# Performance work log

Measured on AMD Instinct MI355X. Metric: run time of the kernel, lower is better.

## Reference

```python
import jax, jax.numpy as jnp
import numpy as np

CONF_THRES = 0.25   # NMS.conf
IOU_THRES = 0.45    # NMS.iou
MAX_NMS = 1024      # fixed candidate count so greedy NMS is jit-compatible
IMG = 640.0


def setup_inputs() -> dict:
    key = jax.random.key(0)
    k0, k1, k2, k3, k4 = jax.random.split(key, 5)
    B, N = 32, 25200
    cxcy = jax.random.uniform(k0, (B, N, 2), dtype=jnp.float32) * IMG
    wh = jax.random.uniform(k1, (B, N, 2), dtype=jnp.float32) * 80.0 + 2.0
    obj = jax.random.uniform(k2, (B, N, 1), dtype=jnp.float32)
    lmk = jax.random.uniform(k3, (B, N, 10), dtype=jnp.float32) * IMG
    cls = jax.random.uniform(k4, (B, N, 1), dtype=jnp.float32)
    # layout: [cx, cy, w, h, obj, 10 landmark coords, 1 class score]
    prediction = jnp.concatenate([cxcy, wh, obj, lmk, cls], axis=2)
    return {"prediction": prediction}


def xywh2xyxy(x):
    cx, cy, w, h = x[:, 0], x[:, 1], x[:, 2], x[:, 3]
    return jnp.stack([cx - w / 2, cy - h / 2, cx + w / 2, cy + h / 2], axis=1)


def pairwise_iou(b):  # b: [K,4] xyxy -> [K,K]
    area = (b[:, 2] - b[:, 0]) * (b[:, 3] - b[:, 1])
    lt = jnp.maximum(b[:, None, :2], b[None, :, :2])
    rb = jnp.minimum(b[:, None, 2:], b[None, :, 2:])
    wh = jnp.clip(rb - lt, 0.0)
    inter = wh[..., 0] * wh[..., 1]
    return inter / (area[:, None] + area[None, :] - inter + 1e-7)


def _nms_image(pred):  # pred: [N,16]
    obj = pred[:, 4]
    score = pred[:, 15] * obj  # x[:,15:] *= x[:,4:5]; nc==1 -> single class, j==0
    valid = (obj > CONF_THRES) & (score > CONF_THRES)  # xc filter + conf filter
    s = jnp.where(valid, score, -1.0)
    top_s, idx = jax.lax.top_k(s, MAX_NMS)  # score-sorted candidates (greedy NMS order)
    x = pred[idx]  # [K,16]
    box = xywh2xyxy(x[:, :4])
    vmask = top_s > 0.0  # valid candidates (invalid slots carry score -1)
    # class offset c = j*4096 is identically 0 since nc==1 -> skip
    iou = pairwise_iou(box)  # [K,K]
    rng = jnp.arange(MAX_NMS)

    def step(keep, i):
        sup = keep[i] & (iou[i] > IOU_THRES) & (rng > i)
        return keep & ~sup, None

    keep, _ = jax.lax.scan(step, vmask, rng)
    det = jnp.concatenate(
        [box, top_s[:, None], x[:, 5:15], jnp.zeros((MAX_NMS, 1), pred.dtype)], axis=1
    )  # [K,16] = box(4) | conf(1) | landmarks(10) | class(1)=0
    return det * keep[:, None].astype(det.dtype), keep


def reference(prediction):
    # Fixed-shape analogue of the per-image ragged output: detections padded to
    # MAX_NMS rows per image (zeroed where suppressed) plus a keep mask.
    det, keep = jax.vmap(_nms_image)(prediction)
    return det, keep
```

## Files before the change

### kernel.cpp

```cpp
#include <hip/hip_runtime.h>
#include <stdint.h>

#define NB 32
#define NN 25200
#define NN4 6300
#define TOPK 1024
#define NF 16
#define CONF 0.25f
#define IOU_T 0.45f
#define NBIN 4096
#define CAP 2048
#define KEY_BASE 0xBE800001u

__device__ __forceinline__ uint32_t score_key(float obj, float cls) {
  float score = __fmul_rn(cls, obj);
  bool valid = (obj > CONF) && (score > CONF);
  float s = valid ? score : -1.0f;
  uint32_t u = __float_as_uint(s);
  return (u & 0x80000000u) ? ~u : (u | 0x80000000u);
}

__device__ __forceinline__ uint64_t shfl_xor_u64(uint64_t v, int m) {
  uint32_t lo = __shfl_xor((uint32_t)v, m, 64);
  uint32_t hi = __shfl_xor((uint32_t)(v >> 32), m, 64);
  return ((uint64_t)hi << 32) | lo;
}

__global__ void k_keys(const float* __restrict__ pred, uint32_t* __restrict__ keys,
                       uint32_t* __restrict__ cnt) {
  if (blockIdx.x == 0 && threadIdx.x < NB) cnt[threadIdx.x] = 0u;
  int g = blockIdx.x * blockDim.x + threadIdx.x;
  if (g >= NB * NN) return;
  const float* row = pred + (size_t)g * NF;
  keys[g] = score_key(row[4], row[15]);
}

__global__ __launch_bounds__(1024) void k_select(const float* __restrict__ pred,
                                                 const uint32_t* __restrict__ keys,
                                                 int* __restrict__ sel,
                                                 float4* __restrict__ boxv,
                                                 float* __restrict__ arv,
                                                 uint32_t* __restrict__ vb) {
  int b = blockIdx.x;
  int tid = threadIdx.x;
  int lane = tid & 63, wid = tid >> 6;
  const uint4* kb4 = (const uint4*)(keys + (size_t)b * NN);
  __shared__ uint32_t hist[NBIN];
  __shared__ uint64_t ent[CAP];
  __shared__ uint32_t wsum[16];
  __shared__ uint32_t sh_bin;
  __shared__ uint32_t sh_cnt;
  #pragma unroll
  for (int k = 0; k < 4; ++k) hist[tid + 1024 * k] = 0;
  ent[tid] = 0; ent[tid + 1024] = 0;
  if (tid == 0) { sh_cnt = 0; sh_bin = 0; }
  __syncthreads();

  uint4 kreg[7];
  #pragma unroll
  for (int k = 0; k < 7; ++k) {
    int i = tid + k * 1024;
    if (i < NN4) {
      kreg[k] = kb4[i];
      uint32_t kv[4] = {kreg[k].x, kreg[k].y, kreg[k].z, kreg[k].w};
      #pragma unroll
      for (int c = 0; c < 4; ++c) {
        uint32_t key = kv[c];
        if (key >= KEY_BASE) {
          uint32_t bin = (key - KEY_BASE) >> 12;
          if (bin > NBIN - 1) bin = NBIN - 1;
          atomicAdd(&hist[bin], 1u);
        }
      }
    }
  }
  __syncthreads();

  uint32_t h[4]; uint32_t s = 0;
  #pragma unroll
  for (int k = 0; k < 4; ++k) { h[k] = hist[NBIN - 1 - (4 * tid + k)]; s += h[k]; }
  uint32_t my = s;
  #pragma unroll
  for (int d = 1; d < 64; d <<= 1) {
    uint32_t v = __shfl_up(s, d, 64);
    if (lane >= d) s += v;
  }
  if (lane == 63) wsum[wid] = s;
  __syncthreads();
  uint32_t base = 0;
  for (int w = 0; w < wid; ++w) base += wsum[w];
  uint32_t cum = base + s - my;
  #pragma unroll
  for (int k = 0; k < 4; ++k) {
    if (cum < TOPK && cum + h[k] >= TOPK) sh_bin = (uint32_t)(NBIN - 1 - (4 * tid + k));
    cum += h[k];
  }
  __syncthreads();
  uint32_t thr = KEY_BASE + (sh_bin << 12);

  #pragma unroll
  for (int k = 0; k < 7; ++k) {
    int i = tid + k * 1024;
    if (i < NN4) {
      uint32_t kv[4] = {kreg[k].x, kreg[k].y, kreg[k].z, kreg[k].w};
      #pragma unroll
      for (int c = 0; c < 4; ++c) {
        uint32_t key = kv[c];
        if (key >= thr) {
          uint32_t p = atomicAdd(&sh_cnt, 1u);
          if (p < CAP) ent[p] = ((uint64_t)key << 32) | (uint32_t)(~(uint32_t)(4 * i + c));
        }
      }
    }
  }
  __syncthreads();

  uint64_t v0 = ent[tid], v1 = ent[tid + 1024];
  for (unsigned kk = 2; kk <= CAP; kk <<= 1) {
    for (unsigned j = kk >> 1; j > 0; j >>= 1) {
      if (j == 1024) {
        uint64_t mx = v0 > v1 ? v0 : v1;
        uint64_t mn = v0 > v1 ? v1 : v0;
        v0 = mx; v1 = mn;
      } else if (j >= 64) {
        __syncthreads();
        ent[tid] = v0; ent[tid + 1024] = v1;
        __syncthreads();
        uint64_t p0 = ent[tid ^ j], p1 = ent[(tid ^ j) + 1024];
        bool low = ((tid & j) == 0);
        bool d0 = ((tid & kk) == 0);
        bool d1 = (((tid + 1024) & kk) == 0);
        v0 = (low != d0) ? (v0 < p0 ? v0 : p0) : (v0 > p0 ? v0 : p0);
        v1 = (low != d1) ? (v1 < p1 ? v1 : p1) : (v1 > p1 ? v1 : p1);
      } else {
        uint64_t p0 = shfl_xor_u64(v0, (int)j);
        uint64_t p1 = shfl_xor_u64(v1, (int)j);
        bool low = ((tid & j) == 0);
        bool d0 = ((tid & kk) == 0);
        bool d1 = (((tid + 1024) & kk) == 0);
        v0 = (low != d0) ? (v0 < p0 ? v0 : p0) : (v0 > p0 ? v0 : p0);
        v1 = (low != d1) ? (v1 < p1 ? v1 : p1) : (v1 > p1 ? v1 : p1);
      }
    }
  }
  uint32_t key = (uint32_t)(v0 >> 32);
  uint32_t n = ~(uint32_t)(v0 & 0xFFFFFFFFu);
  if (n >= NN) n = 0;
  sel[(size_t)b * TOPK + tid] = (int)n;

  bool valid = key >= KEY_BASE;
  uint64_t bal = __ballot(valid);
  if (lane == 0) {
    vb[(size_t)b * 32 + 2 * wid] = (uint32_t)bal;
    vb[(size_t)b * 32 + 2 * wid + 1] = (uint32_t)(bal >> 32);
  }

  {
    const float4* row = (const float4*)(pred + ((size_t)b * NN + n) * NF);
    float4 r0 = row[0];
    float hw = __fmul_rn(r0.z, 0.5f), hh = __fmul_rn(r0.w, 0.5f);
    float x1 = __fsub_rn(r0.x, hw), y1 = __fsub_rn(r0.y, hh);
    float x2 = __fadd_rn(r0.x, hw), y2 = __fadd_rn(r0.y, hh);
    boxv[(size_t)b * TOPK + tid] = make_float4(x1, y1, x2, y2);
    arv[(size_t)b * TOPK + tid] = __fmul_rn(__fsub_rn(x2, x1), __fsub_rn(y2, y1));
  }
}

__global__ __launch_bounds__(1024, 4) void k_maskscan(const float* __restrict__ pred,
                                                      const int* __restrict__ sel,
                                                      const float4* __restrict__ boxv,
                                                      const float* __restrict__ arv,
                                                      const uint32_t* __restrict__ vb,
                                                      uint32_t* __restrict__ mask,
                                                      uint32_t* __restrict__ cnt,
                                                      float* __restrict__ det,
                                                      float* __restrict__ keep_out) {
  int b = blockIdx.x;
  int sblk = blockIdx.y;
  int tid = threadIdx.x;
  int rg = tid & 31;
  int cc = tid >> 5;
  __shared__ uint32_t smask[32 * 1024];
  float* bx1 = (float*)smask;
  float* by1 = bx1 + TOPK;
  float* bx2 = by1 + TOPK;
  float* by2 = bx2 + TOPK;
  float* bar = by2 + TOPK;

  {
    float4 bb = boxv[(size_t)b * TOPK + tid];
    bx1[tid] = bb.x; by1[tid] = bb.y; bx2[tid] = bb.z; by2[tid] = bb.w;
    bar[tid] = arv[(size_t)b * TOPK + tid];
  }
  __syncthreads();
  int i0 = sblk * 128 + rg * 4;
  int iw = i0 >> 5;
  uint32_t wreg[4] = {0u, 0u, 0u, 0u};
  if (cc >= iw) {
    float rx1[4], ry1[4], rx2[4], ry2[4], rar[4];
    #pragma unroll
    for (int k = 0; k < 4; ++k) {
      rx1[k] = bx1[i0 + k]; ry1[k] = by1[i0 + k];
      rx2[k] = bx2[i0 + k]; ry2[k] = by2[i0 + k]; rar[k] = bar[i0 + k];
    }
    for (int jj = 0; jj < 32; ++jj) {
      int j = cc * 32 + jj;
      float cx1 = bx1[j], cy1 = by1[j], cx2 = bx2[j], cy2 = by2[j], car = bar[j];
      #pragma unroll
      for (int k = 0; k < 4; ++k) {
        float lx = fmaxf(rx1[k], cx1);
        float ly = fmaxf(ry1[k], cy1);
        float rx = fminf(rx2[k], cx2);
        float ry = fminf(ry2[k], cy2);
        float wd = fmaxf(__fsub_rn(rx, lx), 0.0f);
        float ht = fmaxf(__fsub_rn(ry, ly), 0.0f);
        float inter = __fmul_rn(wd, ht);
        float den = __fadd_rn(__fsub_rn(__fadd_rn(rar[k], car), inter), 1e-7f);
        float iou = __fdiv_rn(inter, den);
        wreg[k] |= (iou > IOU_T ? 1u : 0u) << jj;
      }
    }
    if (cc == iw) {
      #pragma unroll
      for (int k = 0; k < 4; ++k)
        wreg[k] &= ~((2u << ((i0 + k) & 31)) - 1u);
    }
  }
  uint4 out = make_uint4(wreg[0], wreg[1], wreg[2], wreg[3]);
  *(uint4*)&mask[((size_t)b * 32 + cc) * TOPK + i0] = out;

  __syncthreads();
  if (tid == 0)
    __hip_atomic_fetch_add(&cnt[b], 1u, __ATOMIC_RELEASE, __HIP_MEMORY_SCOPE_AGENT);
  if (sblk != 0) return;

  uint32_t kw0 = 0;
  if (tid < 32) kw0 = vb[(size_t)b * 32 + tid];

  if (tid == 0) {
    while (__hip_atomic_load(&cnt[b], __ATOMIC_RELAXED, __HIP_MEMORY_SCOPE_AGENT) < 8u)
      __builtin_amdgcn_s_sleep(16);
    (void)__hip_atomic_load(&cnt[b], __ATOMIC_ACQUIRE, __HIP_MEMORY_SCOPE_AGENT);
  }
  __syncthreads();

  const uint4* gm4 = (const uint4*)(mask + (size_t)b * (32 * TOPK));
  uint4* sm4 = (uint4*)smask;
  #pragma unroll
  for (int q = 0; q < 8; ++q) {
    int idx4 = tid + q * 1024;
    int row = idx4 >> 8;
    int col4 = idx4 & 255;
    sm4[row * 256 + (col4 ^ (row & 7))] = gm4[idx4];
  }
  __syncthreads();

  if (tid < 32) {
    int l = tid;
    const int rbase = l * 256;
    const int sw = l & 7;
    uint32_t kw = kw0;
    for (int w = 0; w < 32; ++w) {
      uint32_t cur[32];
      #pragma unroll
      for (int q = 0; q < 8; ++q)
        *(uint4*)&cur[4 * q] = sm4[rbase + w * 8 + (q ^ sw)];
      uint32_t rw = kw;
      #pragma unroll
      for (int t = 0; t < 32; ++t)
        if ((rw >> t) & 1u) rw &= ~cur[t];
      uint32_t rf = __shfl(rw, w, 64);
      if (l == w) {
        kw = rf;
      } else if (l > w) {
        uint32_t acc = 0;
        #pragma unroll
        for (int t = 0; t < 32; ++t) acc |= ((rf >> t) & 1u) ? cur[t] : 0u;
        kw &= ~acc;
      }
    }
    smask[l] = kw;
  }
  __syncthreads();

  int n = sel[(size_t)b * TOPK + tid];
  const float4* rowv = (const float4*)(pred + ((size_t)b * NN + n) * NF);
  bool kept = (smask[tid >> 5] >> (tid & 31)) & 1u;
  float m = kept ? 1.0f : 0.0f;
  float4 r0 = rowv[0], r1 = rowv[1], r2 = rowv[2], r3 = rowv[3];
  float score = __fmul_rn(r3.w, r1.x);
  float hw = __fmul_rn(r0.z, 0.5f), hh = __fmul_rn(r0.w, 0.5f);
  float4 o0 = make_float4(__fsub_rn(r0.x, hw) * m, __fsub_rn(r0.y, hh) * m,
                          __fadd_rn(r0.x, hw) * m, __fadd_rn(r0.y, hh) * m);
  float4 o1 = make_float4(score * m, r1.y * m, r1.z * m, r1.w * m);
  float4 o2 = make_float4(r2.x * m, r2.y * m, r2.z * m, r2.w * m);
  float4 o3 = make_float4(r3.x * m, r3.y * m, r3.z * m, 0.0f);
  float4* dst = (float4*)(det + ((size_t)b * TOPK + tid) * NF);
  dst[0] = o0; dst[1] = o1; dst[2] = o2; dst[3] = o3;
  keep_out[(size_t)b * TOPK + tid] = m;
}

extern "C" void kernel_launch(void* const* d_in, const int* in_sizes, int n_in,
                              void* d_out, int out_size, void* d_ws, size_t ws_size,
                              hipStream_t stream) {
  const float* pred = (const float*)d_in[0];
  float* det = (float*)d_out;
  float* keep = det + (size_t)NB * TOPK * NF;

  uint8_t* ws = (uint8_t*)d_ws;
  size_t off = 0;
  uint32_t* keys = (uint32_t*)(ws + off); off += (size_t)NB * NN * 4;
  int* sel = (int*)(ws + off);            off += (size_t)NB * TOPK * 4;
  uint32_t* mask = (uint32_t*)(ws + off); off += (size_t)NB * 32 * TOPK * 4;
  float4* boxv = (float4*)(ws + off);     off += (size_t)NB * TOPK * 16;
  float* arv = (float*)(ws + off);        off += (size_t)NB * TOPK * 4;
  uint32_t* vb = (uint32_t*)(ws + off);   off += (size_t)NB * 32 * 4;
  uint32_t* cnt = (uint32_t*)(ws + off);  off += (size_t)NB * 4;

  k_keys<<<(NB * NN + 255) / 256, 256, 0, stream>>>(pred, keys, cnt);
  k_select<<<NB, 1024, 0, stream>>>(pred, keys, sel, boxv, arv, vb);
  dim3 gm(NB, 8);
  k_maskscan<<<gm, 1024, 0, stream>>>(pred, sel, boxv, arv, vb, mask, cnt, det, keep);
}
```

Baseline: 167.0 us.

## Replace single-warp greedy NMS scan with block-wide fixed-point iteration

The serial 32-lane greedy suppression pass over the bitmask is replaced by a Jacobi-style fixed-point iteration. All 1024 threads OR the rows of currently kept boxes into partial words, a 32-thread reduction updates the keep vector, and the loop repeats until it stops changing. Because suppression only flows from lower to higher index, the greedy result is the only fixed point, so the answer is unchanged. The shared-memory layout switches from an XOR swizzle to a pitch of 257, and the gather of candidate rows from global memory is moved ahead of the spin-wait to overlap its latency. The number of sweeps depends on how deep the suppression chains are, and each sweep costs two block barriers, so data with long chains could be slower than the old scan.

```diff
diff --git a/kernel.cpp b/kernel.cpp
--- a/kernel.cpp
+++ b/kernel.cpp
@@ -11,6 +11,7 @@
 #define NBIN 4096
 #define CAP 2048
 #define KEY_BASE 0xBE800001u
+#define PITCH 257
 
 __device__ __forceinline__ uint32_t score_key(float obj, float cls) {
   float score = __fmul_rn(cls, obj);
@@ -180,8 +181,12 @@
   int tid = threadIdx.x;
   int rg = tid & 31;
   int cc = tid >> 5;
-  __shared__ uint32_t smask[32 * 1024];
-  float* bx1 = (float*)smask;
+  __shared__ uint4 sm4[32 * PITCH];
+  __shared__ uint32_t part[1024];
+  __shared__ uint32_t Kvec[32];
+  __shared__ uint32_t vbs[32];
+  __shared__ uint32_t sflag;
+  float* bx1 = (float*)sm4;
   float* by1 = bx1 + TOPK;
   float* bx2 = by1 + TOPK;
   float* by2 = bx2 + TOPK;
@@ -234,8 +239,9 @@
     __hip_atomic_fetch_add(&cnt[b], 1u, __ATOMIC_RELEASE, __HIP_MEMORY_SCOPE_AGENT);
   if (sblk != 0) return;
 
-  uint32_t kw0 = 0;
-  if (tid < 32) kw0 = vb[(size_t)b * 32 + tid];
+  int n = sel[(size_t)b * TOPK + tid];
+  const float4* rowv = (const float4*)(pred + ((size_t)b * NN + n) * NF);
+  float4 r0 = rowv[0], r1 = rowv[1], r2 = rowv[2], r3 = rowv[3];
 
   if (tid == 0) {
     while (__hip_atomic_load(&cnt[b], __ATOMIC_RELAXED, __HIP_MEMORY_SCOPE_AGENT) < 8u)
@@ -245,49 +251,50 @@
   __syncthreads();
 
   const uint4* gm4 = (const uint4*)(mask + (size_t)b * (32 * TOPK));
-  uint4* sm4 = (uint4*)smask;
   #pragma unroll
   for (int q = 0; q < 8; ++q) {
     int idx4 = tid + q * 1024;
     int row = idx4 >> 8;
     int col4 = idx4 & 255;
-    sm4[row * 256 + (col4 ^ (row & 7))] = gm4[idx4];
-  }
-  __syncthreads();
-
-  if (tid < 32) {
-    int l = tid;
-    const int rbase = l * 256;
-    const int sw = l & 7;
-    uint32_t kw = kw0;
-    for (int w = 0; w < 32; ++w) {
-      uint32_t cur[32];
-      #pragma unroll
-      for (int q = 0; q < 8; ++q)
-        *(uint4*)&cur[4 * q] = sm4[rbase + w * 8 + (q ^ sw)];
-      uint32_t rw = kw;
-      #pragma unroll
-      for (int t = 0; t < 32; ++t)
-        if ((rw >> t) & 1u) rw &= ~cur[t];
-      uint32_t rf = __shfl(rw, w, 64);
-      if (l == w) {
-        kw = rf;
-      } else if (l > w) {
-        uint32_t acc = 0;
+    sm4[row * PITCH + col4] = gm4[idx4];
+  }
+  if (tid < 32) { uint32_t v = vb[(size_t)b * 32 + tid]; vbs[tid] = v; Kvec[tid] = v; }
+  __syncthreads();
+
+  {
+    int l = tid & 31;
+    int chunk = tid >> 5;
+    const int rbase = l * PITCH + chunk * 8;
+    uint32_t go = 1u;
+    for (int sweep = 0; sweep < 1030 && go; ++sweep) {
+      uint32_t kc = Kvec[chunk];
+      uint32_t acc = 0;
+      #pragma unroll
+      for (int q = 0; q < 8; ++q) {
+        uint4 v = sm4[rbase + q];
+        acc |= (0u - ((kc >> (q * 4 + 0)) & 1u)) & v.x;
+        acc |= (0u - ((kc >> (q * 4 + 1)) & 1u)) & v.y;
+        acc |= (0u - ((kc >> (q * 4 + 2)) & 1u)) & v.z;
+        acc |= (0u - ((kc >> (q * 4 + 3)) & 1u)) & v.w;
+      }
+      part[tid] = acc;
+      __syncthreads();
+      if (tid < 32) {
+        uint32_t red = 0;
         #pragma unroll
-        for (int t = 0; t < 32; ++t) acc |= ((rf >> t) & 1u) ? cur[t] : 0u;
-        kw &= ~acc;
-      }
-    }
-    smask[l] = kw;
-  }
-  __syncthreads();
-
-  int n = sel[(size_t)b * TOPK + tid];
-  const float4* rowv = (const float4*)(pred + ((size_t)b * NN + n) * NF);
-  bool kept = (smask[tid >> 5] >> (tid & 31)) & 1u;
+        for (int c = 0; c < 32; ++c) red |= part[c * 32 + tid];
+        uint32_t nk = vbs[tid] & ~red;
+        uint64_t chg = __ballot(nk != Kvec[tid]);
+        Kvec[tid] = nk;
+        if (tid == 0) sflag = (chg != 0ull) ? 1u : 0u;
+      }
+      __syncthreads();
+      go = sflag;
+    }
+  }
+
+  bool kept = (Kvec[tid >> 5] >> (tid & 31)) & 1u;
   float m = kept ? 1.0f : 0.0f;
-  float4 r0 = rowv[0], r1 = rowv[1], r2 = rowv[2], r3 = rowv[3];
   float score = __fmul_rn(r3.w, r1.x);
   float hw = __fmul_rn(r0.z, 0.5f), hh = __fmul_rn(r0.w, 0.5f);
   float4 o0 = make_float4(__fsub_rn(r0.x, hw) * m, __fsub_rn(r0.y, hh) * m,
```

Result: faster. 145.7 us (-12.8%).
